# Kernel tuning notes

Hardware: AMD Instinct MI355X
Metric: run time of the kernel (lower is better)

Reference implementation:

```python
import jax, jax.numpy as jnp
import numpy as np

D_K, D_MODEL, NUM_HEADS = 64, 1024, 16


def _xavier(key, shape):
    # xavier_uniform over last two dims (fan_in=shape[-2], fan_out=shape[-1])
    fan_in, fan_out = shape[-2], shape[-1]
    limit = float(np.sqrt(6.0 / (fan_in + fan_out)))
    return jax.random.uniform(key, shape, jnp.float32, -limit, limit)


def setup_inputs() -> dict:
    key = jax.random.key(0)
    kx, kq, kk, kv, ko = jax.random.split(key, 5)
    x = jax.random.normal(kx, (2, 2048, D_MODEL), dtype=jnp.float32)
    w_q = _xavier(kq, (NUM_HEADS, D_MODEL, D_K))
    w_k = _xavier(kk, (NUM_HEADS, D_MODEL, D_K))
    w_v = _xavier(kv, (NUM_HEADS, D_MODEL, D_K))
    w_o = _xavier(ko, (NUM_HEADS * D_K, D_MODEL))
    return {"x": x, "w_q": w_q, "w_k": w_k, "w_v": w_v, "w_o": w_o}


def reference(x, w_q, w_k, w_v, w_o):
    scale = 1.0 / jnp.sqrt(jnp.asarray(D_K, dtype=jnp.float32))
    q = jnp.einsum('bsd,hdk->bhsk', x, w_q)
    k = jnp.einsum('bsd,hdk->bhsk', x, w_k)
    v = jnp.einsum('bsd,hdk->bhsk', x, w_v)
    scores = jnp.einsum('bhqk,bhmk->bhqm', q, k) * scale  # [B,H,S,S]
    weights = jax.nn.softmax(scores, axis=-1)
    z = jnp.einsum('bhqm,bhmk->bhqk', weights, v)
    b, h, s, dk = z.shape
    z = jnp.transpose(z, (0, 2, 1, 3)).reshape(b, s, h * dk)
    z = jnp.einsum('bse,ed->bsd', z, w_o)
    return x + z  # dropout_prob=0.0 (eval): identity
```

## Files before the change

### kernel.cpp

```cpp
#include <hip/hip_runtime.h>
#include <hip/hip_bf16.h>
#include <stdint.h>

typedef float    f32x4  __attribute__((ext_vector_type(4)));
typedef __bf16   bf16x8 __attribute__((ext_vector_type(8)));
typedef __bf16   bf16x2 __attribute__((ext_vector_type(2)));
typedef uint16_t u16;

#define NHEADS 16
#define DKV    64
#define DMODEL 1024
#define BATCH  2
#define SEQ    2048
#define ROWS   4096

#define EXP2F(x) __builtin_amdgcn_exp2f(x)

__device__ __forceinline__ u16 f2bf(float f) {
  __bf16 h = (__bf16)f;
  union { __bf16 h; u16 u; } c; c.h = h; return c.u;
}
__device__ __forceinline__ uint32_t pk2(float a, float b) {
  union { bf16x2 v; uint32_t u; } c;
  c.v = (bf16x2){(__bf16)a, (__bf16)b};
  return c.u;
}

__device__ __forceinline__ void gload16(const void* g, void* l) {
  __builtin_amdgcn_global_load_lds(
      (const __attribute__((address_space(1))) uint32_t*)g,
      (__attribute__((address_space(3))) uint32_t*)l, 16, 0, 0);
}

__device__ __forceinline__ f32x4 mfma16(bf16x8 a, bf16x8 b, f32x4 c) {
  return __builtin_amdgcn_mfma_f32_16x16x32_bf16(a, b, c, 0, 0, 0);
}

__global__ void prep_kernel(const float* __restrict__ x, u16* __restrict__ xb,
                            const float* __restrict__ wq, const float* __restrict__ wk,
                            const float* __restrict__ wv, const float* __restrict__ wo,
                            u16* __restrict__ wt, u16* __restrict__ wot) {
  int blk = blockIdx.x, tid = threadIdx.x;
  if (blk < 2048) {
    int i = blk * 256 + tid;
    const float4* p = (const float4*)(x + (size_t)i * 8);
    float4 a = p[0], b = p[1];
    uint32_t o0 = pk2(a.x, a.y), o1 = pk2(a.z, a.w);
    uint32_t o2 = pk2(b.x, b.y), o3 = pk2(b.z, b.w);
    uint4 pk = make_uint4(o0, o1, o2, o3);
    *(uint4*)(xb + (size_t)i * 8) = pk;
    return;
  }
  __shared__ float t[64][65];
  int wblk = blk - 2048;
  const float* src; u16* dst; int sld, dld;
  if (wblk < 768) {
    int p = wblk >> 8, rem = wblk & 255;
    int h = rem >> 4, dt = rem & 15;
    const float* w = (p == 0) ? wq : (p == 1) ? wk : wv;
    src = w + ((size_t)h * 1024 + dt * 64) * 64;   sld = 64;
    dst = wt + ((size_t)(p * 1024 + h * 64)) * 1024 + dt * 64; dld = 1024;
  } else {
    int t2 = wblk - 768, rt = t2 >> 4, ct = t2 & 15;
    src = wo + (size_t)(rt * 64) * 1024 + ct * 64;  sld = 1024;
    dst = wot + (size_t)(ct * 64) * 1024 + rt * 64; dld = 1024;
  }
#pragma unroll
  for (int i = 0; i < 16; i++) {
    int e = tid + i * 256, r = e >> 6, c = e & 63;
    t[r][c] = src[(size_t)r * sld + c];
  }
  __syncthreads();
#pragma unroll
  for (int i = 0; i < 16; i++) {
    int e = tid + i * 256, r = e >> 6, c = e & 63;
    dst[(size_t)r * dld + c] = f2bf(t[c][r]);
  }
}

template<int EPI>
__global__ __launch_bounds__(256) void gemm_bt(
    const u16* __restrict__ A, const u16* __restrict__ Bt, int K, int ntn,
    u16* __restrict__ qout, u16* __restrict__ kout, u16* __restrict__ vout,
    const float* __restrict__ xres, float* __restrict__ fout) {
  __shared__ __align__(16) u16 As[128 * 32];
  __shared__ __align__(16) u16 Bs[128 * 32];
  int tid = threadIdx.x, l = tid & 63, w = tid >> 6;
  int nwg = gridDim.x, cpx = nwg >> 3;
  int bid = (blockIdx.x & 7) * cpx + (blockIdx.x >> 3);
  int m0 = (bid / ntn) * 128, n0 = (bid % ntn) * 128;
  int wm = (w >> 1) * 64, wn = (w & 1) * 64;
  int cg = l >> 4, cl = l & 15;
  int lrow = l >> 2, lcol = l & 3;

  f32x4 acc[4][4];
#pragma unroll
  for (int i = 0; i < 4; i++)
#pragma unroll
    for (int j = 0; j < 4; j++) acc[i][j] = (f32x4){0.f, 0.f, 0.f, 0.f};

  for (int k0 = 0; k0 < K; k0 += 32) {
    __syncthreads();
    const u16* ga = A  + (size_t)(m0 + w * 16 + lrow) * K + k0 + lcol * 8;
    const u16* gb = Bt + (size_t)(n0 + w * 16 + lrow) * K + k0 + lcol * 8;
    gload16(ga,            &As[(w * 16) * 32]);
    gload16(ga + 64 * (size_t)K, &As[(w * 16 + 64) * 32]);
    gload16(gb,            &Bs[(w * 16) * 32]);
    gload16(gb + 64 * (size_t)K, &Bs[(w * 16 + 64) * 32]);
    __syncthreads();

    bf16x8 af[4], bfr[4];
#pragma unroll
    for (int mi = 0; mi < 4; mi++)
      af[mi] = *(const bf16x8*)&As[(wm + mi * 16 + cl) * 32 + cg * 8];
#pragma unroll
    for (int ni = 0; ni < 4; ni++)
      bfr[ni] = *(const bf16x8*)&Bs[(wn + ni * 16 + cl) * 32 + cg * 8];
#pragma unroll
    for (int mi = 0; mi < 4; mi++)
#pragma unroll
      for (int ni = 0; ni < 4; ni++)
        acc[mi][ni] = mfma16(af[mi], bfr[ni], acc[mi][ni]);
  }

#pragma unroll
  for (int mi = 0; mi < 4; mi++)
#pragma unroll
    for (int ni = 0; ni < 4; ni++) {
      int nbase = n0 + wn + ni * 16 + cl;
#pragma unroll
      for (int r = 0; r < 4; r++) {
        int m = m0 + wm + mi * 16 + cg * 4 + r;
        float v = acc[mi][ni][r];
        if (EPI == 0) {
          int p = nbase >> 10, hh = (nbase >> 6) & 15, dk = nbase & 63;
          int b = m >> 11, s = m & 2047;
          int bh = b * 16 + hh;
          if (p == 2) {
            vout[((size_t)bh * 64 + dk) * 2048 + s] = f2bf(v);
          } else {
            size_t o = ((size_t)bh * 2048 + s) * 64 + dk;
            u16* dst = (p == 0) ? qout : kout;
            dst[o] = f2bf((p == 0) ? v * 0.18033688f : v);
          }
        } else {
          size_t o = (size_t)m * 1024 + nbase;
          fout[o] = v + xres[o];
        }
      }
    }
}

__global__ __launch_bounds__(512) void attn_kernel(
    const u16* __restrict__ q, const u16* __restrict__ k,
    const u16* __restrict__ vt, u16* __restrict__ z) {
  __shared__ __align__(16) u16 Ks[2][64 * 64];
  __shared__ __align__(16) u16 Vs[2][64 * 64];
  __shared__ __align__(16) u16 Ps[8][16 * 64];
  int tid = threadIdx.x, l = tid & 63, w = tid >> 6;
  int blk = blockIdx.x;
  int xcd = blk & 7, slot = blk >> 3;
  int bh = xcd + 8 * (slot >> 4), qt = slot & 15;
  int b = bh >> 4, h = bh & 15;
  int q0 = qt * 128 + w * 16;
  int cg = l >> 4, cl = l & 15;
  int swz = (cl & 7) << 4;

  const u16* qb = q  + ((size_t)bh * 2048 + q0) * 64;
  const u16* kb = k  + (size_t)bh * 2048 * 64;
  const u16* vb = vt + (size_t)bh * 64 * 2048;

  int srow = w * 8 + (l >> 3);
  int scb  = (l & 7) ^ (l >> 3);

  bf16x8 bq0 = *(const bf16x8*)&qb[(size_t)cl * 64 + cg * 8];
  bf16x8 bq1 = *(const bf16x8*)&qb[(size_t)cl * 64 + 32 + cg * 8];

  f32x4 oacc[4];
#pragma unroll
  for (int i = 0; i < 4; i++) oacc[i] = (f32x4){0.f, 0.f, 0.f, 0.f};
  float mrun = -3.0e38f, lrun = 0.f;

  gload16(kb + (size_t)srow * 64 + scb * 8,   &Ks[0][(w * 8) * 64]);
  gload16(vb + (size_t)srow * 2048 + scb * 8, &Vs[0][(w * 8) * 64]);
  __syncthreads();

  for (int t = 0; t < 32; t++) {
    int cur = t & 1, nxt = cur ^ 1;
    if (t + 1 < 32) {
      gload16(kb + ((size_t)(t + 1) * 64 + srow) * 64 + scb * 8,  &Ks[nxt][(w * 8) * 64]);
      gload16(vb + (size_t)srow * 2048 + (t + 1) * 64 + scb * 8,  &Vs[nxt][(w * 8) * 64]);
    }

    f32x4 sc[4];
    __builtin_amdgcn_s_setprio(1);
#pragma unroll
    for (int g = 0; g < 4; g++) {
      const char* kp = (const char*)&Ks[cur][(g * 16 + cl) * 64];
      bf16x8 a0 = *(const bf16x8*)(kp + ((cg * 16)      ^ swz));
      bf16x8 a1 = *(const bf16x8*)(kp + ((cg * 16 + 64) ^ swz));
      f32x4 t2 = (f32x4){0.f, 0.f, 0.f, 0.f};
      t2 = mfma16(a0, bq0, t2);
      t2 = mfma16(a1, bq1, t2);
      sc[g] = t2;
    }
    __builtin_amdgcn_s_setprio(0);

    float m01 = fmaxf(fmaxf(sc[0][0], sc[0][1]), fmaxf(sc[0][2], sc[0][3]));
    float m23 = fmaxf(fmaxf(sc[1][0], sc[1][1]), fmaxf(sc[1][2], sc[1][3]));
    float m45 = fmaxf(fmaxf(sc[2][0], sc[2][1]), fmaxf(sc[2][2], sc[2][3]));
    float m67 = fmaxf(fmaxf(sc[3][0], sc[3][1]), fmaxf(sc[3][2], sc[3][3]));
    float mx = fmaxf(fmaxf(m01, m23), fmaxf(m45, m67));
    mx = fmaxf(mx, __shfl_xor(mx, 16));
    mx = fmaxf(mx, __shfl_xor(mx, 32));
    if (!__all(mx <= mrun + 8.0f)) {
      float mnew = fmaxf(mrun, mx);
      float fac = EXP2F(mrun - mnew);
      mrun = mnew;
      lrun *= fac;
#pragma unroll
      for (int nd = 0; nd < 4; nd++)
#pragma unroll
        for (int r = 0; r < 4; r++) oacc[nd][r] *= fac;
    }
    float rs = 0.f;
#pragma unroll
    for (int g = 0; g < 4; g++)
#pragma unroll
      for (int r = 0; r < 4; r++) {
        float p = EXP2F(sc[g][r] - mrun);
        sc[g][r] = p;
        rs += p;
      }
    rs += __shfl_xor(rs, 16);
    rs += __shfl_xor(rs, 32);
    lrun += rs;

    char* pw = (char*)&Ps[w][cl * 64];
#pragma unroll
    for (int g = 0; g < 4; g++) {
      uint32_t lo = pk2(sc[g][0], sc[g][1]);
      uint32_t hi = pk2(sc[g][2], sc[g][3]);
      *(uint2*)(pw + ((g * 32 + cg * 8) ^ swz)) = make_uint2(lo, hi);
    }
    bf16x8 pb0 = *(const bf16x8*)(pw + ((cg * 16)      ^ swz));
    bf16x8 pb1 = *(const bf16x8*)(pw + ((cg * 16 + 64) ^ swz));

    __builtin_amdgcn_s_setprio(1);
#pragma unroll
    for (int nd = 0; nd < 4; nd++) {
      const char* vp = (const char*)&Vs[cur][(nd * 16 + cl) * 64];
      bf16x8 v0 = *(const bf16x8*)(vp + ((cg * 16)      ^ swz));
      bf16x8 v1 = *(const bf16x8*)(vp + ((cg * 16 + 64) ^ swz));
      oacc[nd] = mfma16(v0, pb0, oacc[nd]);
      oacc[nd] = mfma16(v1, pb1, oacc[nd]);
    }
    __builtin_amdgcn_s_setprio(0);

    __syncthreads();
  }

  float inv = 1.0f / lrun;
  u16* zb = z + ((size_t)(b * 2048) + q0) * 1024 + h * 64;
#pragma unroll
  for (int nd = 0; nd < 4; nd++) {
    uint32_t lo = pk2(oacc[nd][0] * inv, oacc[nd][1] * inv);
    uint32_t hi = pk2(oacc[nd][2] * inv, oacc[nd][3] * inv);
    *(uint2*)&zb[(size_t)cl * 1024 + nd * 16 + cg * 4] = make_uint2(lo, hi);
  }
}

extern "C" void kernel_launch(void* const* d_in, const int* in_sizes, int n_in,
                              void* d_out, int out_size, void* d_ws, size_t ws_size,
                              hipStream_t stream) {
  const float* x  = (const float*)d_in[0];
  const float* wq = (const float*)d_in[1];
  const float* wk = (const float*)d_in[2];
  const float* wv = (const float*)d_in[3];
  const float* wo = (const float*)d_in[4];
  float* out = (float*)d_out;

  uint8_t* ws = (uint8_t*)d_ws;
  u16* xb  = (u16*)(ws);
  u16* wt  = (u16*)(ws + (8ull  << 20));
  u16* wot = (u16*)(ws + (14ull << 20));
  u16* qb  = (u16*)(ws + (16ull << 20));
  u16* kb  = (u16*)(ws + (24ull << 20));
  u16* vt  = (u16*)(ws + (32ull << 20));
  u16* zb  = (u16*)(ws + (40ull << 20));
  if (ws_size < (48ull << 20)) return;

  prep_kernel<<<3072, 256, 0, stream>>>(x, xb, wq, wk, wv, wo, wt, wot);
  gemm_bt<0><<<768, 256, 0, stream>>>(xb, wt, 1024, 24, qb, kb, vt, nullptr, nullptr);
  attn_kernel<<<512, 512, 0, stream>>>(qb, kb, vt, zb);
  gemm_bt<1><<<256, 256, 0, stream>>>(zb, wot, 1024, 8, nullptr, nullptr, nullptr, x, out);
}
```

Before: 207.6 us.

## Split V projection into transposed GEMM and use narrower tiles for output GEMM

The QKV projection is split in two. Q and K use the existing GEMM, and V is computed as a separate GEMM with swapped operands (Wv^T times x^T). This writes V^T with coalesced row-major stores in place of the strided transposed scatter. The GEMM kernel gains a template N-tile width, and the output projection moves to 128x64 tiles so 512 workgroups launch instead of 256. This adds a kernel launch and uses smaller tiles with less reuse per block, in exchange for better coalescing and higher occupancy across CUs.

```diff
diff --git a/kernel.cpp b/kernel.cpp
--- a/kernel.cpp
+++ b/kernel.cpp
@@ -78,55 +78,56 @@
   }
 }
 
-template<int EPI>
+template<int EPI, int NT>
 __global__ __launch_bounds__(256) void gemm_bt(
     const u16* __restrict__ A, const u16* __restrict__ Bt, int K, int ntn,
     u16* __restrict__ qout, u16* __restrict__ kout, u16* __restrict__ vout,
     const float* __restrict__ xres, float* __restrict__ fout) {
   __shared__ __align__(16) u16 As[128 * 32];
-  __shared__ __align__(16) u16 Bs[128 * 32];
+  __shared__ __align__(16) u16 Bs[NT * 32 * 32];
   int tid = threadIdx.x, l = tid & 63, w = tid >> 6;
   int nwg = gridDim.x, cpx = nwg >> 3;
   int bid = (blockIdx.x & 7) * cpx + (blockIdx.x >> 3);
-  int m0 = (bid / ntn) * 128, n0 = (bid % ntn) * 128;
-  int wm = (w >> 1) * 64, wn = (w & 1) * 64;
+  int m0 = (bid / ntn) * 128, n0 = (bid % ntn) * (NT * 32);
+  int wm = (w >> 1) * 64, wn = (w & 1) * (NT * 16);
   int cg = l >> 4, cl = l & 15;
   int lrow = l >> 2, lcol = l & 3;
 
-  f32x4 acc[4][4];
+  f32x4 acc[4][NT];
 #pragma unroll
   for (int i = 0; i < 4; i++)
 #pragma unroll
-    for (int j = 0; j < 4; j++) acc[i][j] = (f32x4){0.f, 0.f, 0.f, 0.f};
+    for (int j = 0; j < NT; j++) acc[i][j] = (f32x4){0.f, 0.f, 0.f, 0.f};
 
   for (int k0 = 0; k0 < K; k0 += 32) {
     __syncthreads();
     const u16* ga = A  + (size_t)(m0 + w * 16 + lrow) * K + k0 + lcol * 8;
     const u16* gb = Bt + (size_t)(n0 + w * 16 + lrow) * K + k0 + lcol * 8;
-    gload16(ga,            &As[(w * 16) * 32]);
+    gload16(ga,                  &As[(w * 16) * 32]);
     gload16(ga + 64 * (size_t)K, &As[(w * 16 + 64) * 32]);
-    gload16(gb,            &Bs[(w * 16) * 32]);
-    gload16(gb + 64 * (size_t)K, &Bs[(w * 16 + 64) * 32]);
+#pragma unroll
+    for (int rr = 0; rr < NT / 2; rr++)
+      gload16(gb + (size_t)rr * 64 * K, &Bs[(w * 16 + rr * 64) * 32]);
     __syncthreads();
 
-    bf16x8 af[4], bfr[4];
+    bf16x8 af[4], bfr[NT];
 #pragma unroll
     for (int mi = 0; mi < 4; mi++)
       af[mi] = *(const bf16x8*)&As[(wm + mi * 16 + cl) * 32 + cg * 8];
 #pragma unroll
-    for (int ni = 0; ni < 4; ni++)
+    for (int ni = 0; ni < NT; ni++)
       bfr[ni] = *(const bf16x8*)&Bs[(wn + ni * 16 + cl) * 32 + cg * 8];
 #pragma unroll
     for (int mi = 0; mi < 4; mi++)
 #pragma unroll
-      for (int ni = 0; ni < 4; ni++)
+      for (int ni = 0; ni < NT; ni++)
         acc[mi][ni] = mfma16(af[mi], bfr[ni], acc[mi][ni]);
   }
 
 #pragma unroll
   for (int mi = 0; mi < 4; mi++)
 #pragma unroll
-    for (int ni = 0; ni < 4; ni++) {
+    for (int ni = 0; ni < NT; ni++) {
       int nbase = n0 + wn + ni * 16 + cl;
 #pragma unroll
       for (int r = 0; r < 4; r++) {
@@ -136,13 +137,11 @@
           int p = nbase >> 10, hh = (nbase >> 6) & 15, dk = nbase & 63;
           int b = m >> 11, s = m & 2047;
           int bh = b * 16 + hh;
-          if (p == 2) {
-            vout[((size_t)bh * 64 + dk) * 2048 + s] = f2bf(v);
-          } else {
-            size_t o = ((size_t)bh * 2048 + s) * 64 + dk;
-            u16* dst = (p == 0) ? qout : kout;
-            dst[o] = f2bf((p == 0) ? v * 0.18033688f : v);
-          }
+          size_t o = ((size_t)bh * 2048 + s) * 64 + dk;
+          u16* dst = (p == 0) ? qout : kout;
+          dst[o] = f2bf((p == 0) ? v * 0.18033688f : v);
+        } else if (EPI == 2) {
+          vout[(size_t)m * 4096 + nbase] = f2bf(v);
         } else {
           size_t o = (size_t)m * 1024 + nbase;
           fout[o] = v + xres[o];
@@ -168,7 +167,7 @@
 
   const u16* qb = q  + ((size_t)bh * 2048 + q0) * 64;
   const u16* kb = k  + (size_t)bh * 2048 * 64;
-  const u16* vb = vt + (size_t)bh * 64 * 2048;
+  const u16* vb = vt + (size_t)(h * 64) * 4096 + b * 2048;
 
   int srow = w * 8 + (l >> 3);
   int scb  = (l & 7) ^ (l >> 3);
@@ -182,14 +181,14 @@
   float mrun = -3.0e38f, lrun = 0.f;
 
   gload16(kb + (size_t)srow * 64 + scb * 8,   &Ks[0][(w * 8) * 64]);
-  gload16(vb + (size_t)srow * 2048 + scb * 8, &Vs[0][(w * 8) * 64]);
+  gload16(vb + (size_t)srow * 4096 + scb * 8, &Vs[0][(w * 8) * 64]);
   __syncthreads();
 
   for (int t = 0; t < 32; t++) {
     int cur = t & 1, nxt = cur ^ 1;
     if (t + 1 < 32) {
-      gload16(kb + ((size_t)(t + 1) * 64 + srow) * 64 + scb * 8,  &Ks[nxt][(w * 8) * 64]);
-      gload16(vb + (size_t)srow * 2048 + (t + 1) * 64 + scb * 8,  &Vs[nxt][(w * 8) * 64]);
+      gload16(kb + ((size_t)(t + 1) * 64 + srow) * 64 + scb * 8,   &Ks[nxt][(w * 8) * 64]);
+      gload16(vb + (size_t)srow * 4096 + (t + 1) * 64 + scb * 8,   &Vs[nxt][(w * 8) * 64]);
     }
 
     f32x4 sc[4];
@@ -290,8 +289,11 @@
   u16* zb  = (u16*)(ws + (40ull << 20));
   if (ws_size < (48ull << 20)) return;
 
+  const u16* wtv = wt + (size_t)2048 * 1024;
+
   prep_kernel<<<3072, 256, 0, stream>>>(x, xb, wq, wk, wv, wo, wt, wot);
-  gemm_bt<0><<<768, 256, 0, stream>>>(xb, wt, 1024, 24, qb, kb, vt, nullptr, nullptr);
+  gemm_bt<0, 4><<<512, 256, 0, stream>>>(xb, wt, 1024, 16, qb, kb, nullptr, nullptr, nullptr);
+  gemm_bt<2, 2><<<512, 256, 0, stream>>>(wtv, xb, 1024, 64, nullptr, nullptr, vt, nullptr, nullptr);
   attn_kernel<<<512, 512, 0, stream>>>(qb, kb, vt, zb);
-  gemm_bt<1><<<256, 256, 0, stream>>>(zb, wot, 1024, 8, nullptr, nullptr, nullptr, x, out);
-}
+  gemm_bt<1, 2><<<512, 256, 0, stream>>>(zb, wot, 1024, 16, nullptr, nullptr, nullptr, x, out);
+}
```

Result: slower. 218.2 us (+5.1%).
